# Kernel tuning notes

Measured on AMD Instinct MI355X. Metric: run time of the kernel, lower is better.

The kernel has to match this reference:

```python
import jax, jax.numpy as jnp
import numpy as np

MARGIN = 1.0  # init kwarg 'margin'
NUM_CLASSES = 16


def setup_inputs() -> dict:
    key = jax.random.key(0)
    k1, k2 = jax.random.split(key)
    embeddings = jax.random.normal(k1, (384, 1024), dtype=jnp.float32)
    labels = jax.random.randint(k2, (384,), 0, NUM_CLASSES, dtype=jnp.int64)
    return {"embeddings": embeddings, "labels": labels}


def reference(embeddings, labels):
    # Dense, on-device equivalent of the CPU triplet mining:
    # valid triplet (a, p, n) iff labels[a]==labels[p], a<p, labels[n]!=labels[a].
    # Mean over all valid triplets == original torch losses.mean().
    B = embeddings.shape[0]
    sq = jnp.sum(embeddings * embeddings, axis=1)                      # [B]
    # Squared pairwise distances via Gram matrix (same math as (x_i-x_j)^2.sum())
    D = sq[:, None] + sq[None, :] - 2.0 * (embeddings @ embeddings.T)  # [B,B]

    eq = labels[:, None] == labels[None, :]                            # same-label mask [B,B]
    idx = jnp.arange(B)
    ap_valid = eq & (idx[:, None] < idx[None, :])                      # anchor<positive pairs
    mask = ap_valid[:, :, None] & (~eq)[:, None, :]                    # [a,p,n] valid triplets

    # loss[a,p,n] = relu(D[a,p] - D[a,n] + margin)
    loss = jax.nn.relu(D[:, :, None] - D[:, None, :] + MARGIN)         # [B,B,B]

    count = jnp.sum(mask)
    total = jnp.sum(jnp.where(mask, loss, jnp.float32(0.0)))
    mean = jnp.where(count > 0, total / count.astype(loss.dtype), jnp.float32(0.0))
    return mean, count
```

## Files before the change

### kernel.cpp

```cpp
#include <hip/hip_runtime.h>


constexpr int BN  = 384;
constexpr int DIM = 1024;
constexpr float MARGIN = 1.0f;
constexpr int LDK = 68;

__global__ __launch_bounds__(256) void gram_kernel(
    const float* __restrict__ E, float* __restrict__ P,
    float* __restrict__ sqpart, float* __restrict__ total,
    int* __restrict__ cnt, int* __restrict__ ticket, int KC, int NZ) {
    __shared__ float Ast[32 * LDK];
    __shared__ float Bst[32 * LDK];
    const int t    = threadIdx.x;
    const int tile = blockIdx.x % 36;
    const int z    = blockIdx.x / 36;
    const int ti   = tile / 6, tj = tile % 6;
    const int i0   = ti * 64, j0 = tj * 64;

    if (blockIdx.x == 0 && t == 0) { *total = 0.f; *cnt = 0; *ticket = 0; }

    const int r  = t >> 2;
    const int kq = t & 3;
    const int kb = kq * 8;
    const int rs = r ^ (kq << 4);

    const float* Ab = E + (size_t)(i0 + r) * DIM + z * KC + kb;
    const float* Bb = E + (size_t)(j0 + r) * DIM + z * KC + kb;

    float4 a0 = *(const float4*)(Ab);
    float4 a1 = *(const float4*)(Ab + 4);
    float4 b0 = *(const float4*)(Bb);
    float4 b1 = *(const float4*)(Bb + 4);

    const int tx = t & 15, ty = t >> 4;
    float acc[4][4] = {};

    for (int kt = 0; kt < KC; kt += 32) {
        Ast[(kb + 0) * LDK + rs] = a0.x; Ast[(kb + 1) * LDK + rs] = a0.y;
        Ast[(kb + 2) * LDK + rs] = a0.z; Ast[(kb + 3) * LDK + rs] = a0.w;
        Ast[(kb + 4) * LDK + rs] = a1.x; Ast[(kb + 5) * LDK + rs] = a1.y;
        Ast[(kb + 6) * LDK + rs] = a1.z; Ast[(kb + 7) * LDK + rs] = a1.w;
        Bst[(kb + 0) * LDK + rs] = b0.x; Bst[(kb + 1) * LDK + rs] = b0.y;
        Bst[(kb + 2) * LDK + rs] = b0.z; Bst[(kb + 3) * LDK + rs] = b0.w;
        Bst[(kb + 4) * LDK + rs] = b1.x; Bst[(kb + 5) * LDK + rs] = b1.y;
        Bst[(kb + 6) * LDK + rs] = b1.z; Bst[(kb + 7) * LDK + rs] = b1.w;
        __syncthreads();
        if (kt + 32 < KC) {
            a0 = *(const float4*)(Ab + kt + 32);
            a1 = *(const float4*)(Ab + kt + 36);
            b0 = *(const float4*)(Bb + kt + 32);
            b1 = *(const float4*)(Bb + kt + 36);
        }
#pragma unroll
        for (int kk = 0; kk < 32; ++kk) {
            const int sw = (kk >> 3) << 4;
            const float4 av = *(const float4*)&Ast[kk * LDK + ((4 * ty) ^ sw)];
            const float4 bv = *(const float4*)&Bst[kk * LDK + ((4 * tx) ^ sw)];
            const float aa[4] = {av.x, av.y, av.z, av.w};
            const float bb[4] = {bv.x, bv.y, bv.z, bv.w};
#pragma unroll
            for (int i2 = 0; i2 < 4; ++i2)
#pragma unroll
                for (int j2 = 0; j2 < 4; ++j2)
                    acc[i2][j2] += aa[i2] * bb[j2];
        }
        __syncthreads();
    }

    const size_t rowstride = (size_t)NZ * BN;
#pragma unroll
    for (int i2 = 0; i2 < 4; ++i2) {
        *(float4*)&P[(size_t)(i0 + 4 * ty + i2) * rowstride + (size_t)z * BN + (j0 + 4 * tx)] =
            make_float4(acc[i2][0], acc[i2][1], acc[i2][2], acc[i2][3]);
    }
    if (ti == tj && tx == ty) {
#pragma unroll
        for (int i2 = 0; i2 < 4; ++i2)
            sqpart[z * BN + (i0 + 4 * ty + i2)] = acc[i2][i2];
    }
}

template <int NZ>
__global__ __launch_bounds__(128) void triplet_kernel(
    const float* __restrict__ P, const float* __restrict__ sqpart,
    const int* __restrict__ labels, float* __restrict__ total,
    int* __restrict__ cnt, int* __restrict__ ticket, float* __restrict__ out) {
    __shared__ float Hrow[BN];
    __shared__ int   lab[BN];
    __shared__ int   poslist[BN];
    __shared__ int   npos_s;
    __shared__ float wsum[2];
    __shared__ int   wcnt[2];
    const int a   = blockIdx.x;
    const int tid = threadIdx.x;

    if (tid == 0) npos_s = 0;
    for (int i = tid; i < BN; i += 128) lab[i] = labels[i];

    if (tid < 96) {
        const int c0 = tid * 4;
        float4 g = make_float4(0.f, 0.f, 0.f, 0.f);
        float4 s = make_float4(0.f, 0.f, 0.f, 0.f);
#pragma unroll
        for (int z = 0; z < NZ; ++z) {
            const float4 pv = *(const float4*)&P[(size_t)a * ((size_t)NZ * BN) + z * BN + c0];
            const float4 sv = *(const float4*)&sqpart[z * BN + c0];
            g.x += pv.x; g.y += pv.y; g.z += pv.z; g.w += pv.w;
            s.x += sv.x; s.y += sv.y; s.z += sv.z; s.w += sv.w;
        }
        Hrow[c0 + 0] = s.x - 2.f * g.x;
        Hrow[c0 + 1] = s.y - 2.f * g.y;
        Hrow[c0 + 2] = s.z - 2.f * g.z;
        Hrow[c0 + 3] = s.w - 2.f * g.w;
    }
    __syncthreads();

    const int la = lab[a];
    int lc = 0;
#pragma unroll
    for (int q = 0; q < 3; ++q) {
        const int p = tid + q * 128;
        if (lab[p] != la) ++lc;
        else if (p > a) { const int k = atomicAdd(&npos_s, 1); poslist[k] = p; }
    }
    __syncthreads();
    const int np = npos_s;

    const float hn0 = Hrow[tid];
    const float hn1 = Hrow[tid + 128];
    const float hn2 = Hrow[tid + 256];
    const bool  ng0 = (lab[tid]       != la);
    const bool  ng1 = (lab[tid + 128] != la);
    const bool  ng2 = (lab[tid + 256] != la);

    float ls = 0.f;
    for (int k = 0; k < np; ++k) {
        const float dpm = Hrow[poslist[k]] + MARGIN;
        if (ng0) { const float v = dpm - hn0; ls += (v > 0.f) ? v : 0.f; }
        if (ng1) { const float v = dpm - hn1; ls += (v > 0.f) ? v : 0.f; }
        if (ng2) { const float v = dpm - hn2; ls += (v > 0.f) ? v : 0.f; }
    }

#pragma unroll
    for (int off = 32; off; off >>= 1) {
        ls += __shfl_down(ls, off);
        lc += __shfl_down(lc, off);
    }
    const int wave = tid >> 6, lane = tid & 63;
    if (lane == 0) { wsum[wave] = ls; wcnt[wave] = lc; }
    __syncthreads();
    if (tid == 0) {
        const float s    = wsum[0] + wsum[1];
        const int   nneg = wcnt[0] + wcnt[1];
        if (s != 0.f) atomicAdd(total, s);
        if (np)       atomicAdd(cnt, np * nneg);
        __threadfence();
        const int done = atomicAdd(ticket, 1);
        if (done == (int)gridDim.x - 1) {
            const float tot = atomicAdd(total, 0.0f);
            const int   c   = atomicAdd(cnt, 0);
            out[0] = (c > 0) ? tot / (float)c : 0.f;
            out[1] = (float)c;
        }
    }
}

extern "C" void kernel_launch(void* const* d_in, const int* in_sizes, int n_in,
                              void* d_out, int out_size, void* d_ws, size_t ws_size,
                              hipStream_t stream) {
    const float* E      = (const float*)d_in[0];
    const int*   labels = (const int*)d_in[1];
    float*       out    = (float*)d_out;

    int Z = 1;
    for (int cand : {8, 4, 2}) {
        size_t need = (size_t)cand * BN * BN * 4 + (size_t)cand * BN * 4 + 64;
        if (need <= ws_size) { Z = cand; break; }
    }

    char*  ws     = (char*)d_ws;
    float* P      = (float*)ws;
    float* sqpart = (float*)(ws + (size_t)Z * BN * BN * 4);
    float* total  = (float*)(ws + (size_t)Z * BN * BN * 4 + (size_t)Z * BN * 4);
    int*   cnt    = (int*)(total + 1);
    int*   ticket = (int*)(total + 2);

    gram_kernel<<<36 * Z, 256, 0, stream>>>(E, P, sqpart, total, cnt, ticket, DIM / Z, Z);

    switch (Z) {
        case 8:  triplet_kernel<8><<<BN, 128, 0, stream>>>(P, sqpart, labels, total, cnt, ticket, out); break;
        case 4:  triplet_kernel<4><<<BN, 128, 0, stream>>>(P, sqpart, labels, total, cnt, ticket, out); break;
        case 2:  triplet_kernel<2><<<BN, 128, 0, stream>>>(P, sqpart, labels, total, cnt, ticket, out); break;
        default: triplet_kernel<1><<<BN, 128, 0, stream>>>(P, sqpart, labels, total, cnt, ticket, out); break;
    }
}
```

Baseline: 83.06 us.

## Fuse Gram computation into per-anchor triplet blocks with deterministic final reduction

Replaces the split-K tiled Gram kernel plus per-anchor triplet kernel with one fused kernel. Each block handles three anchors and computes their distance rows directly from global memory with dot products, so no partial Gram matrix is written to or read from workspace. Global atomics and the ticket scheme give way to per-block partial sums reduced by a small finalize kernel, and the negative count comes from a label histogram. Every block re-reads the whole embedding matrix, so the Gram reuse is lost and the kernel leans on L2 bandwidth instead of shared-memory tiling.

```diff
diff --git a/kernel.cpp b/kernel.cpp
--- a/kernel.cpp
+++ b/kernel.cpp
@@ -1,168 +1,136 @@
 #include <hip/hip_runtime.h>
 
 
-constexpr int BN  = 384;
-constexpr int DIM = 1024;
+constexpr int   BN     = 384;
+constexpr int   DIM    = 1024;
+constexpr int   NCH    = DIM / 4;
 constexpr float MARGIN = 1.0f;
-constexpr int LDK = 68;
+constexpr int   APB    = 3;
+constexpr int   NBLK   = BN / APB;
+constexpr int   NTHR   = 2 * BN;
 
-__global__ __launch_bounds__(256) void gram_kernel(
-    const float* __restrict__ E, float* __restrict__ P,
-    float* __restrict__ sqpart, float* __restrict__ total,
-    int* __restrict__ cnt, int* __restrict__ ticket, int KC, int NZ) {
-    __shared__ float Ast[32 * LDK];
-    __shared__ float Bst[32 * LDK];
-    const int t    = threadIdx.x;
-    const int tile = blockIdx.x % 36;
-    const int z    = blockIdx.x / 36;
-    const int ti   = tile / 6, tj = tile % 6;
-    const int i0   = ti * 64, j0 = tj * 64;
+__global__ __launch_bounds__(NTHR) void fused_kernel(
+    const float* __restrict__ E, const int* __restrict__ labels,
+    float* __restrict__ wsum, int* __restrict__ wcnt) {
 
-    if (blockIdx.x == 0 && t == 0) { *total = 0.f; *cnt = 0; *ticket = 0; }
+    __shared__ float Hs[APB][BN];
+    __shared__ float Pp[APB][BN];
+    __shared__ int   poslist[APB][BN];
+    __shared__ int   npos[APB];
+    __shared__ int   hist[16];
+    __shared__ float wred[NTHR / 64];
 
-    const int r  = t >> 2;
-    const int kq = t & 3;
-    const int kb = kq * 8;
-    const int rs = r ^ (kq << 4);
+    const int tid = threadIdx.x;
+    const int a0  = blockIdx.x * APB;
+    const int r   = tid >> 1;
+    const int h   = tid & 1;
 
-    const float* Ab = E + (size_t)(i0 + r) * DIM + z * KC + kb;
-    const float* Bb = E + (size_t)(j0 + r) * DIM + z * KC + kb;
+    const int la0 = labels[a0 + 0];
+    const int la1 = labels[a0 + 1];
+    const int la2 = labels[a0 + 2];
 
-    float4 a0 = *(const float4*)(Ab);
-    float4 a1 = *(const float4*)(Ab + 4);
-    float4 b0 = *(const float4*)(Bb);
-    float4 b1 = *(const float4*)(Bb + 4);
+    if (tid < 16)  hist[tid] = 0;
+    if (tid < APB) npos[tid] = 0;
+    __syncthreads();
 
-    const int tx = t & 15, ty = t >> 4;
-    float acc[4][4] = {};
-
-    for (int kt = 0; kt < KC; kt += 32) {
-        Ast[(kb + 0) * LDK + rs] = a0.x; Ast[(kb + 1) * LDK + rs] = a0.y;
-        Ast[(kb + 2) * LDK + rs] = a0.z; Ast[(kb + 3) * LDK + rs] = a0.w;
-        Ast[(kb + 4) * LDK + rs] = a1.x; Ast[(kb + 5) * LDK + rs] = a1.y;
-        Ast[(kb + 6) * LDK + rs] = a1.z; Ast[(kb + 7) * LDK + rs] = a1.w;
-        Bst[(kb + 0) * LDK + rs] = b0.x; Bst[(kb + 1) * LDK + rs] = b0.y;
-        Bst[(kb + 2) * LDK + rs] = b0.z; Bst[(kb + 3) * LDK + rs] = b0.w;
-        Bst[(kb + 4) * LDK + rs] = b1.x; Bst[(kb + 5) * LDK + rs] = b1.y;
-        Bst[(kb + 6) * LDK + rs] = b1.z; Bst[(kb + 7) * LDK + rs] = b1.w;
-        __syncthreads();
-        if (kt + 32 < KC) {
-            a0 = *(const float4*)(Ab + kt + 32);
-            a1 = *(const float4*)(Ab + kt + 36);
-            b0 = *(const float4*)(Bb + kt + 32);
-            b1 = *(const float4*)(Bb + kt + 36);
-        }
-#pragma unroll
-        for (int kk = 0; kk < 32; ++kk) {
-            const int sw = (kk >> 3) << 4;
-            const float4 av = *(const float4*)&Ast[kk * LDK + ((4 * ty) ^ sw)];
-            const float4 bv = *(const float4*)&Bst[kk * LDK + ((4 * tx) ^ sw)];
-            const float aa[4] = {av.x, av.y, av.z, av.w};
-            const float bb[4] = {bv.x, bv.y, bv.z, bv.w};
-#pragma unroll
-            for (int i2 = 0; i2 < 4; ++i2)
-#pragma unroll
-                for (int j2 = 0; j2 < 4; ++j2)
-                    acc[i2][j2] += aa[i2] * bb[j2];
-        }
-        __syncthreads();
+    int lj = 0;
+    if (tid < BN) {
+        lj = labels[tid];
+        atomicAdd(&hist[lj], 1);
+        if (lj == la0 && tid > a0 + 0) poslist[0][atomicAdd(&npos[0], 1)] = tid;
+        if (lj == la1 && tid > a0 + 1) poslist[1][atomicAdd(&npos[1], 1)] = tid;
+        if (lj == la2 && tid > a0 + 2) poslist[2][atomicAdd(&npos[2], 1)] = tid;
     }
 
-    const size_t rowstride = (size_t)NZ * BN;
+    const float4* ej = (const float4*)(E + (size_t)r * DIM);
+    const float4* e0 = (const float4*)(E + (size_t)(a0 + 0) * DIM);
+    const float4* e1 = (const float4*)(E + (size_t)(a0 + 1) * DIM);
+    const float4* e2 = (const float4*)(E + (size_t)(a0 + 2) * DIM);
+
+    float d0 = 0.f, d1 = 0.f, d2 = 0.f, qs = 0.f;
+#pragma unroll 4
+    for (int c = h; c < NCH; c += 2) {
+        const float4 v = ej[c];
+        const float4 x = e0[c];
+        const float4 y = e1[c];
+        const float4 z = e2[c];
+        qs = fmaf(v.w, v.w, fmaf(v.z, v.z, fmaf(v.y, v.y, fmaf(v.x, v.x, qs))));
+        d0 = fmaf(v.w, x.w, fmaf(v.z, x.z, fmaf(v.y, x.y, fmaf(v.x, x.x, d0))));
+        d1 = fmaf(v.w, y.w, fmaf(v.z, y.z, fmaf(v.y, y.y, fmaf(v.x, y.x, d1))));
+        d2 = fmaf(v.w, z.w, fmaf(v.z, z.z, fmaf(v.y, z.y, fmaf(v.x, z.x, d2))));
+    }
+    d0 += __shfl_xor(d0, 1);
+    d1 += __shfl_xor(d1, 1);
+    d2 += __shfl_xor(d2, 1);
+    qs += __shfl_xor(qs, 1);
+    if (h == 0) {
+        Hs[0][r] = fmaf(-2.f, d0, qs);
+        Hs[1][r] = fmaf(-2.f, d1, qs);
+        Hs[2][r] = fmaf(-2.f, d2, qs);
+    }
+    __syncthreads();
+
+    if (tid < BN) {
 #pragma unroll
-    for (int i2 = 0; i2 < 4; ++i2) {
-        *(float4*)&P[(size_t)(i0 + 4 * ty + i2) * rowstride + (size_t)z * BN + (j0 + 4 * tx)] =
-            make_float4(acc[i2][0], acc[i2][1], acc[i2][2], acc[i2][3]);
+        for (int i = 0; i < APB; ++i)
+            if (tid < npos[i]) Pp[i][tid] = Hs[i][poslist[i][tid]] + MARGIN;
     }
-    if (ti == tj && tx == ty) {
+    __syncthreads();
+
+    float ls = 0.f;
+    if (tid < BN) {
+        const int las[APB] = {la0, la1, la2};
 #pragma unroll
-        for (int i2 = 0; i2 < 4; ++i2)
-            sqpart[z * BN + (i0 + 4 * ty + i2)] = acc[i2][i2];
+        for (int i = 0; i < APB; ++i) {
+            if (lj != las[i]) {
+                const float hn = Hs[i][tid];
+                const int   np = npos[i];
+                for (int k = 0; k < np; ++k) {
+                    const float v = Pp[i][k] - hn;
+                    ls += (v > 0.f) ? v : 0.f;
+                }
+            }
+        }
+    }
+
+#pragma unroll
+    for (int off = 32; off; off >>= 1) ls += __shfl_down(ls, off);
+    if ((tid & 63) == 0) wred[tid >> 6] = ls;
+    __syncthreads();
+    if (tid == 0) {
+        float s = 0.f;
+#pragma unroll
+        for (int w = 0; w < NTHR / 64; ++w) s += wred[w];
+        const int c = npos[0] * (BN - hist[la0]) +
+                      npos[1] * (BN - hist[la1]) +
+                      npos[2] * (BN - hist[la2]);
+        wsum[blockIdx.x] = s;
+        wcnt[blockIdx.x] = c;
     }
 }
 
-template <int NZ>
-__global__ __launch_bounds__(128) void triplet_kernel(
-    const float* __restrict__ P, const float* __restrict__ sqpart,
-    const int* __restrict__ labels, float* __restrict__ total,
-    int* __restrict__ cnt, int* __restrict__ ticket, float* __restrict__ out) {
-    __shared__ float Hrow[BN];
-    __shared__ int   lab[BN];
-    __shared__ int   poslist[BN];
-    __shared__ int   npos_s;
-    __shared__ float wsum[2];
-    __shared__ int   wcnt[2];
-    const int a   = blockIdx.x;
-    const int tid = threadIdx.x;
-
-    if (tid == 0) npos_s = 0;
-    for (int i = tid; i < BN; i += 128) lab[i] = labels[i];
-
-    if (tid < 96) {
-        const int c0 = tid * 4;
-        float4 g = make_float4(0.f, 0.f, 0.f, 0.f);
-        float4 s = make_float4(0.f, 0.f, 0.f, 0.f);
-#pragma unroll
-        for (int z = 0; z < NZ; ++z) {
-            const float4 pv = *(const float4*)&P[(size_t)a * ((size_t)NZ * BN) + z * BN + c0];
-            const float4 sv = *(const float4*)&sqpart[z * BN + c0];
-            g.x += pv.x; g.y += pv.y; g.z += pv.z; g.w += pv.w;
-            s.x += sv.x; s.y += sv.y; s.z += sv.z; s.w += sv.w;
-        }
-        Hrow[c0 + 0] = s.x - 2.f * g.x;
-        Hrow[c0 + 1] = s.y - 2.f * g.y;
-        Hrow[c0 + 2] = s.z - 2.f * g.z;
-        Hrow[c0 + 3] = s.w - 2.f * g.w;
-    }
-    __syncthreads();
-
-    const int la = lab[a];
-    int lc = 0;
-#pragma unroll
-    for (int q = 0; q < 3; ++q) {
-        const int p = tid + q * 128;
-        if (lab[p] != la) ++lc;
-        else if (p > a) { const int k = atomicAdd(&npos_s, 1); poslist[k] = p; }
-    }
-    __syncthreads();
-    const int np = npos_s;
-
-    const float hn0 = Hrow[tid];
-    const float hn1 = Hrow[tid + 128];
-    const float hn2 = Hrow[tid + 256];
-    const bool  ng0 = (lab[tid]       != la);
-    const bool  ng1 = (lab[tid + 128] != la);
-    const bool  ng2 = (lab[tid + 256] != la);
-
-    float ls = 0.f;
-    for (int k = 0; k < np; ++k) {
-        const float dpm = Hrow[poslist[k]] + MARGIN;
-        if (ng0) { const float v = dpm - hn0; ls += (v > 0.f) ? v : 0.f; }
-        if (ng1) { const float v = dpm - hn1; ls += (v > 0.f) ? v : 0.f; }
-        if (ng2) { const float v = dpm - hn2; ls += (v > 0.f) ? v : 0.f; }
-    }
-
+__global__ __launch_bounds__(NBLK) void finalize_kernel(
+    const float* __restrict__ wsum, const int* __restrict__ wcnt,
+    float* __restrict__ out) {
+    __shared__ float fs[NBLK / 64];
+    __shared__ int   fc[NBLK / 64];
+    const int t = threadIdx.x;
+    float s = wsum[t];
+    int   c = wcnt[t];
 #pragma unroll
     for (int off = 32; off; off >>= 1) {
-        ls += __shfl_down(ls, off);
-        lc += __shfl_down(lc, off);
+        s += __shfl_down(s, off);
+        c += __shfl_down(c, off);
     }
-    const int wave = tid >> 6, lane = tid & 63;
-    if (lane == 0) { wsum[wave] = ls; wcnt[wave] = lc; }
+    if ((t & 63) == 0) { fs[t >> 6] = s; fc[t >> 6] = c; }
     __syncthreads();
-    if (tid == 0) {
-        const float s    = wsum[0] + wsum[1];
-        const int   nneg = wcnt[0] + wcnt[1];
-        if (s != 0.f) atomicAdd(total, s);
-        if (np)       atomicAdd(cnt, np * nneg);
-        __threadfence();
-        const int done = atomicAdd(ticket, 1);
-        if (done == (int)gridDim.x - 1) {
-            const float tot = atomicAdd(total, 0.0f);
-            const int   c   = atomicAdd(cnt, 0);
-            out[0] = (c > 0) ? tot / (float)c : 0.f;
-            out[1] = (float)c;
-        }
+    if (t == 0) {
+        float tot = 0.f;
+        int   cnt = 0;
+#pragma unroll
+        for (int w = 0; w < NBLK / 64; ++w) { tot += fs[w]; cnt += fc[w]; }
+        out[0] = (cnt > 0) ? tot / (float)cnt : 0.f;
+        out[1] = (float)cnt;
     }
 }
 
@@ -173,25 +141,9 @@
     const int*   labels = (const int*)d_in[1];
     float*       out    = (float*)d_out;
 
-    int Z = 1;
-    for (int cand : {8, 4, 2}) {
-        size_t need = (size_t)cand * BN * BN * 4 + (size_t)cand * BN * 4 + 64;
-        if (need <= ws_size) { Z = cand; break; }
-    }
+    float* wsum = (float*)d_ws;
+    int*   wcnt = (int*)((char*)d_ws + (size_t)NBLK * sizeof(float));
 
-    char*  ws     = (char*)d_ws;
-    float* P      = (float*)ws;
-    float* sqpart = (float*)(ws + (size_t)Z * BN * BN * 4);
-    float* total  = (float*)(ws + (size_t)Z * BN * BN * 4 + (size_t)Z * BN * 4);
-    int*   cnt    = (int*)(total + 1);
-    int*   ticket = (int*)(total + 2);
-
-    gram_kernel<<<36 * Z, 256, 0, stream>>>(E, P, sqpart, total, cnt, ticket, DIM / Z, Z);
-
-    switch (Z) {
-        case 8:  triplet_kernel<8><<<BN, 128, 0, stream>>>(P, sqpart, labels, total, cnt, ticket, out); break;
-        case 4:  triplet_kernel<4><<<BN, 128, 0, stream>>>(P, sqpart, labels, total, cnt, ticket, out); break;
-        case 2:  triplet_kernel<2><<<BN, 128, 0, stream>>>(P, sqpart, labels, total, cnt, ticket, out); break;
-        default: triplet_kernel<1><<<BN, 128, 0, stream>>>(P, sqpart, labels, total, cnt, ticket, out); break;
-    }
+    fused_kernel<<<NBLK, NTHR, 0, stream>>>(E, labels, wsum, wcnt);
+    finalize_kernel<<<1, NBLK, 0, stream>>>(wsum, wcnt, out);
 }
```

Result: slower. 121.6 us (+46.4%).
